# Performance work log

Hardware: AMD Instinct MI355X
Metric: run time of the kernel (lower is better)

The kernel has to match this reference:

```python
import jax, jax.numpy as jnp
import numpy as np

B, T, C = 4, 2048, 1024
H = 16
HS = C // H  # 64

def setup_inputs() -> dict:
    key = jax.random.key(0)
    k1, k2, k3, k4 = jax.random.split(key, 4)
    scale = 0.02
    return {
        "x": jax.random.normal(k1, (B, T, C), dtype=jnp.float32),
        "w_kqv": jax.random.normal(k2, (C, 3 * C), dtype=jnp.float32) * scale,
        "w_proj": jax.random.normal(k3, (C, C), dtype=jnp.float32) * scale,
        "b_proj": jax.random.normal(k4, (C,), dtype=jnp.float32) * scale,
    }

def reference(x, w_kqv, w_proj, b_proj):
    b, t, c = x.shape
    qkv = x @ w_kqv                       # [B,T,3C]
    q, k, v = jnp.split(qkv, 3, axis=-1)
    def heads(a):
        return a.reshape(b, t, H, HS).transpose(0, 2, 1, 3)  # [B,H,T,HS]
    q, k, v = heads(q), heads(k), heads(v)
    # faithful to source: scores MULTIPLIED by sqrt(head_size)
    scores = jnp.einsum('bhqd,bhkd->bhqk', q, k) * (HS ** 0.5)
    mask = jnp.tril(jnp.ones((t, t), dtype=bool))
    scores = jnp.where(mask[None, None], scores, -jnp.inf)
    attn = jax.nn.softmax(scores, axis=-1)
    out = jnp.einsum('bhqk,bhkd->bhqd', attn, v)  # [B,H,T,HS]
    out = out.transpose(0, 2, 1, 3).reshape(b, t, c)
    return out @ w_proj + b_proj
```

## Files before the change

### kernel.cpp

```cpp
#include <hip/hip_runtime.h>
#include <hip/hip_bf16.h>
#include <cstdint>

#define BB 4
#define TT 2048
#define CC 1024
#define HH 16
#define HS 64
#define MM (BB*TT)

#define QSCALE 11.5415603629f

typedef _Float16 f16;
typedef _Float16 f16x8 __attribute__((ext_vector_type(8)));
typedef _Float16 f16x4 __attribute__((ext_vector_type(4)));
typedef float f32x4 __attribute__((ext_vector_type(4)));
typedef float f32x16 __attribute__((ext_vector_type(16)));

#define MFMA16(a,b,c) __builtin_amdgcn_mfma_f32_16x16x32_f16(a,b,c,0,0,0)
#define MFMA32(a,b,c) __builtin_amdgcn_mfma_f32_32x32x16_f16(a,b,c,0,0,0)

__device__ __forceinline__ void g2lds16(void* lds, const void* g) {
  __builtin_amdgcn_global_load_lds(
      (const __attribute__((address_space(1))) void*)g,
      (__attribute__((address_space(3))) void*)lds, 16, 0, 0);
}

__device__ __forceinline__ int pk2(float a, float b) {
  auto r = __builtin_amdgcn_cvt_pkrtz(a, b);
  return __builtin_bit_cast(int, r);
}

union U8 { int4 i; f16x8 h; };

__global__ __launch_bounds__(256) void cvt_kernel(const float* __restrict__ in,
                                                  f16* __restrict__ out, int n4) {
  int i = blockIdx.x * blockDim.x + threadIdx.x;
  if (i < n4) {
    float4 v = ((const float4*)in)[i];
    f16x4 o;
    o[0] = (f16)v.x; o[1] = (f16)v.y; o[2] = (f16)v.z; o[3] = (f16)v.w;
    ((f16x4*)out)[i] = o;
  }
}

__global__ __launch_bounds__(256) void transpose_cvt(const float* __restrict__ in,
                                                     f16* __restrict__ out,
                                                     int K, int N) {
  __shared__ float tile[32][33];
  int n0 = blockIdx.x * 32, k0 = blockIdx.y * 32;
  int tx = threadIdx.x, ty = threadIdx.y;
  #pragma unroll
  for (int i = 0; i < 32; i += 8)
    tile[ty + i][tx] = in[(size_t)(k0 + ty + i) * N + n0 + tx];
  __syncthreads();
  #pragma unroll
  for (int i = 0; i < 32; i += 8)
    out[(size_t)(n0 + ty + i) * K + k0 + tx] = (f16)tile[tx][ty + i];
}

__device__ __forceinline__ void gstage(const f16* __restrict__ A,
                                       const f16* __restrict__ Bt,
                                       f16* as, f16* bs,
                                       int row0, int col0, int kt, int t) {
  const int K = 1024;
  #pragma unroll
  for (int i = 0; i < 2; ++i) {
    int off = i * 8192 + t * 16;
    int row = off >> 7;
    int cbB = off & 127;
    int scb = cbB ^ ((row & 7) << 4);
    g2lds16((char*)as + off, (const char*)(A  + (size_t)(row0 + row) * K + kt) + scb);
    g2lds16((char*)bs + off, (const char*)(Bt + (size_t)(col0 + row) * K + kt) + scb);
  }
}

template<int EPI>
__global__ __launch_bounds__(512) void gemm_bt(const f16* __restrict__ A,
                                               const f16* __restrict__ Bt,
                                               f16* __restrict__ qT,
                                               f16* __restrict__ kT,
                                               f16* __restrict__ vT,
                                               const float* __restrict__ bias,
                                               float* __restrict__ outF) {
  const int K = 1024;
  __shared__ f16 As[2][128 * 64];
  __shared__ f16 Bs[2][128 * 64];
  const int t = threadIdx.x;
  const int l = t & 63, w = t >> 6;
  const int lr = l & 15, lh = l >> 4;
  const int row0 = blockIdx.y * 128, col0 = blockIdx.x * 128;
  const int wm = w >> 2, wn = w & 3;
  const int wr = wm * 64, wc = wn * 32;
  const int sx = (lr & 7) << 4;

  f32x4 acc[4][2] = {};

  gstage(A, Bt, As[0], Bs[0], row0, col0, 0, t);
  int buf = 0;
  for (int kt = 0; kt < K; kt += 64) {
    asm volatile("" ::: "memory");
    const bool pf = (kt + 64) < K;
    if (pf) gstage(A, Bt, As[buf ^ 1], Bs[buf ^ 1], row0, col0, kt + 64, t);
    if (pf) asm volatile("s_waitcnt vmcnt(4)" ::: "memory");
    else    asm volatile("s_waitcnt vmcnt(0)" ::: "memory");
    __builtin_amdgcn_sched_barrier(0);
    __builtin_amdgcn_s_barrier();
    const char* as = (const char*)As[buf];
    const char* bs = (const char*)Bs[buf];
    __builtin_amdgcn_s_setprio(1);
    #pragma unroll
    for (int kk = 0; kk < 64; kk += 32) {
      f16x8 af[4], bfr[2];
      #pragma unroll
      for (int m = 0; m < 4; ++m)
        af[m]  = *(const f16x8*)(as + (wr + m * 16 + lr) * 128
                                    + ((kk * 2 + lh * 16) ^ sx));
      #pragma unroll
      for (int n = 0; n < 2; ++n)
        bfr[n] = *(const f16x8*)(bs + (wc + n * 16 + lr) * 128
                                    + ((kk * 2 + lh * 16) ^ sx));
      #pragma unroll
      for (int m = 0; m < 4; ++m)
        #pragma unroll
        for (int n = 0; n < 2; ++n)
          acc[m][n] = MFMA16(af[m], bfr[n], acc[m][n]);
    }
    __builtin_amdgcn_s_setprio(0);
    __builtin_amdgcn_sched_barrier(0);
    __builtin_amdgcn_s_barrier();
    buf ^= 1;
  }

  #pragma unroll
  for (int m = 0; m < 4; ++m) {
    #pragma unroll
    for (int n = 0; n < 2; ++n) {
      #pragma unroll
      for (int j = 0; j < 4; ++j) {
        float val = acc[m][n][j];
        int gr = row0 + wr + m * 16 + lh * 4 + j;
        int gc = col0 + wc + n * 16 + lr;
        if (EPI == 0) {
          int which = gc >> 10;
          int c = gc & 1023;
          int h = c >> 6, d = c & 63;
          int b = gr >> 11, tt = gr & 2047;
          size_t bh = (size_t)(b * HH + h);
          if (which == 0)      qT[(bh * TT + tt) * HS + d] = (f16)(val * QSCALE);
          else if (which == 1) kT[(bh * TT + tt) * HS + d] = (f16)val;
          else                 vT[(bh * HS + d) * TT + tt] = (f16)val;
        } else {
          outF[(size_t)gr * CC + gc] = val + bias[gc];
        }
      }
    }
  }
}

template<bool MASKED>
__device__ __forceinline__ void step32L(
    int kglob, int qa, int l31, int hi,
    const f16* __restrict__ ks, const f16* __restrict__ vs, int kbs,
    const f16x8 (&qf)[4],
    float& m, f32x4& lv, f32x16& oA, f32x16& oB) {
  const int sx = (l31 & 7) << 4;
  const char* krow = (const char*)(ks + (kbs + l31) * 64);
  f32x16 sa = {}, sb = {};
  {
    f16x8 kf0 = *(const f16x8*)(krow + ((0 * 32 + hi * 16) ^ sx));
    f16x8 kf1 = *(const f16x8*)(krow + ((1 * 32 + hi * 16) ^ sx));
    f16x8 kf2 = *(const f16x8*)(krow + ((2 * 32 + hi * 16) ^ sx));
    f16x8 kf3 = *(const f16x8*)(krow + ((3 * 32 + hi * 16) ^ sx));
    sa = MFMA32(kf0, qf[0], sa);
    sb = MFMA32(kf2, qf[2], sb);
    sa = MFMA32(kf1, qf[1], sa);
    sb = MFMA32(kf3, qf[3], sb);
  }
  float p[16];
  #pragma unroll
  for (int r = 0; r < 16; ++r) {
    float sv = sa[r] + sb[r];
    if (MASKED) {
      int k = kglob + (r & 3) + 8 * (r >> 2) + 4 * hi;
      p[r] = (k <= qa) ? sv : -INFINITY;
    } else p[r] = sv;
  }
  float t0 = fmaxf(fmaxf(p[0], p[1]), fmaxf(p[2], p[3]));
  float t1 = fmaxf(fmaxf(p[4], p[5]), fmaxf(p[6], p[7]));
  float t2 = fmaxf(fmaxf(p[8], p[9]), fmaxf(p[10], p[11]));
  float t3 = fmaxf(fmaxf(p[12], p[13]), fmaxf(p[14], p[15]));
  float mx = fmaxf(fmaxf(t0, t1), fmaxf(t2, t3));
  if (__any(mx > m + 14.0f)) {
    mx = fmaxf(mx, __shfl_xor(mx, 32));
    float mn = fmaxf(m, mx);
    float corr = __builtin_amdgcn_exp2f(m - mn);
    m = mn;
    #pragma unroll
    for (int r = 0; r < 4; ++r) lv[r] *= corr;
    #pragma unroll
    for (int r = 0; r < 16; ++r) { oA[r] *= corr; oB[r] *= corr; }
  }
  #pragma unroll
  for (int r = 0; r < 16; ++r) {
    p[r] = __builtin_amdgcn_exp2f(p[r] - m);
    lv[r & 3] += p[r];
  }
  int pkv[8];
  #pragma unroll
  for (int j = 0; j < 8; ++j) pkv[j] = pk2(p[2 * j], p[2 * j + 1]);
  int e0 = pkv[0], e2 = pkv[2];
  asm("v_permlane32_swap_b32 %0, %1" : "+v"(e0), "+v"(e2));
  int e1 = pkv[1], e3 = pkv[3];
  asm("v_permlane32_swap_b32 %0, %1" : "+v"(e1), "+v"(e3));
  int f0 = pkv[4], f2 = pkv[6];
  asm("v_permlane32_swap_b32 %0, %1" : "+v"(f0), "+v"(f2));
  int f1 = pkv[5], f3 = pkv[7];
  asm("v_permlane32_swap_b32 %0, %1" : "+v"(f1), "+v"(f3));
  U8 b0, b1;
  b0.i = (int4){ e0, e1, e2, e3 };
  b1.i = (int4){ f0, f1, f2, f3 };
  const char* vrow0 = (const char*)(vs + l31 * 64);
  const char* vrow1 = (const char*)(vs + (l31 + 32) * 64);
  const int kc0 = (kbs * 2 + hi * 16) ^ sx;
  const int kc1 = (kbs * 2 + hi * 16 + 32) ^ sx;
  f16x8 v00 = *(const f16x8*)(vrow0 + kc0);
  f16x8 v01 = *(const f16x8*)(vrow0 + kc1);
  f16x8 v10 = *(const f16x8*)(vrow1 + kc0);
  f16x8 v11 = *(const f16x8*)(vrow1 + kc1);
  oA = MFMA32(v00, b0.h, oA);
  oA = MFMA32(v01, b1.h, oA);
  oB = MFMA32(v10, b0.h, oB);
  oB = MFMA32(v11, b1.h, oB);
}

__device__ __forceinline__ void stage_tile(const f16* __restrict__ Kb,
                                           const f16* __restrict__ Vb,
                                           f16* ks, f16* vs,
                                           int kb, int w, int l) {
  #pragma unroll
  for (int j = 0; j < 2; ++j) {
    int off = w * 2048 + j * 1024 + l * 16;
    int row = off >> 7;
    int cb  = off & 127;
    int scb = cb ^ ((row & 7) << 4);
    g2lds16((char*)ks + off, (const char*)(Kb + (size_t)(kb + row) * HS) + scb);
    g2lds16((char*)vs + off, (const char*)(Vb + (size_t)row * TT + kb) + scb);
  }
}

__global__ __launch_bounds__(256) void attn_kernel(const f16* __restrict__ qT,
                                                   const f16* __restrict__ kT,
                                                   const f16* __restrict__ vT,
                                                   f16* __restrict__ aout) {
  const int bh = blockIdx.x;
  const int pr = blockIdx.y;
  const int t = threadIdx.x, l = t & 63, w = t >> 6;
  const int l31 = l & 31, hi = l >> 5;
  const f16* __restrict__ Qb = qT + (size_t)bh * TT * HS;
  const f16* __restrict__ Kb = kT + (size_t)bh * TT * HS;
  const f16* __restrict__ Vb = vT + (size_t)bh * HS * TT;
  const int b = bh >> 4, h = bh & 15;

  __shared__ f16 Ks[2][64 * 64];
  __shared__ f16 Vs[2][64 * 64];

  #pragma unroll
  for (int ph = 0; ph < 2; ++ph) {
    const int qb = ph ? pr : (15 - pr);
    const int q0w = qb * 128 + w * 32;
    const int qa = q0w + l31;

    f16x8 qf[4];
    #pragma unroll
    for (int j = 0; j < 4; ++j)
      qf[j] = *(const f16x8*)&Qb[(size_t)qa * HS + 16 * j + hi * 8];

    float m = -INFINITY;
    f32x4 lv = {};
    f32x16 oA = {}, oB = {};

    const int nt = 2 * qb + 2;
    stage_tile(Kb, Vb, Ks[0], Vs[0], 0, w, l);
    __syncthreads();
    int buf = 0;
    for (int ti = 0; ti < nt; ++ti) {
      if (ti + 1 < nt)
        stage_tile(Kb, Vb, Ks[buf ^ 1], Vs[buf ^ 1], (ti + 1) * 64, w, l);
      const int kb = ti * 64;
      const f16* ks = Ks[buf];
      const f16* vs = Vs[buf];
      if (kb < q0w)
        step32L<false>(kb, qa, l31, hi, ks, vs, 0, qf, m, lv, oA, oB);
      else if (kb == q0w)
        step32L<true >(kb, qa, l31, hi, ks, vs, 0, qf, m, lv, oA, oB);
      if (kb + 32 < q0w)
        step32L<false>(kb + 32, qa, l31, hi, ks, vs, 32, qf, m, lv, oA, oB);
      else if (kb + 32 == q0w)
        step32L<true >(kb + 32, qa, l31, hi, ks, vs, 32, qf, m, lv, oA, oB);
      __syncthreads();
      buf ^= 1;
    }

    float lsum = (lv[0] + lv[1]) + (lv[2] + lv[3]);
    lsum += __shfl_xor(lsum, 32);
    float li = 1.0f / lsum;

    f16* orow = aout + (size_t)(b * TT + qa) * CC + h * HS;
    #pragma unroll
    for (int rq = 0; rq < 4; ++rq) {
      f16x4 o4a, o4b;
      #pragma unroll
      for (int j = 0; j < 4; ++j) {
        int r = rq * 4 + j;
        o4a[j] = (f16)(oA[r] * li);
        o4b[j] = (f16)(oB[r] * li);
      }
      int dA = 8 * rq + 4 * hi;
      *(f16x4*)&orow[dA]      = o4a;
      *(f16x4*)&orow[32 + dA] = o4b;
    }
    __syncthreads();
  }
}

extern "C" void kernel_launch(void* const* d_in, const int* in_sizes, int n_in,
                              void* d_out, int out_size, void* d_ws, size_t ws_size,
                              hipStream_t stream) {
  const float* x      = (const float*)d_in[0];
  const float* w_kqv  = (const float*)d_in[1];
  const float* w_proj = (const float*)d_in[2];
  const float* b_proj = (const float*)d_in[3];
  float* out = (float*)d_out;

  char* ws = (char*)d_ws;
  f16* xb    = (f16*)(ws);
  f16* wkqvT = (f16*)(ws + 16777216);
  f16* wpT   = (f16*)(ws + 23068672);
  f16* qT    = (f16*)(ws + 25165824);
  f16* kT    = (f16*)(ws + 41943040);
  f16* vT    = (f16*)(ws + 58720256);
  f16* aout  = (f16*)(ws + 75497472);

  cvt_kernel<<<8192, 256, 0, stream>>>(x, xb, (MM * CC) / 4);
  transpose_cvt<<<dim3(3 * CC / 32, CC / 32), dim3(32, 8), 0, stream>>>(w_kqv, wkqvT, CC, 3 * CC);
  transpose_cvt<<<dim3(CC / 32, CC / 32), dim3(32, 8), 0, stream>>>(w_proj, wpT, CC, CC);

  gemm_bt<0><<<dim3(3 * CC / 128, MM / 128), 512, 0, stream>>>(xb, wkqvT, qT, kT, vT, nullptr, nullptr);

  attn_kernel<<<dim3(BB * HH, 8), 256, 0, stream>>>(qT, kT, vT, aout);

  gemm_bt<1><<<dim3(CC / 128, MM / 128), 512, 0, stream>>>(aout, wpT, nullptr, nullptr, nullptr, b_proj, out);
}
```

Before: 212.4 us.

## Split attention KV tiles across two wave groups and merge softmax partials in LDS

The attention kernel now runs 512 threads per block. Two groups of four waves each handle one 32-key half of every 64-key tile for the same query rows, and staging is split across all eight waves. At the end, the second group writes its partial output, max and sum to LDS, and the first group merges them flash-decoding style before writing. This doubles the waves per block to raise parallelism and latency hiding (the grid is only 512 blocks). In exchange it adds an LDS merge step, an extra barrier, and a shared union buffer.

```diff
diff --git a/kernel.cpp b/kernel.cpp
--- a/kernel.cpp
+++ b/kernel.cpp
@@ -234,41 +234,48 @@
   oB = MFMA32(v11, b1.h, oB);
 }
 
-__device__ __forceinline__ void stage_tile(const f16* __restrict__ Kb,
-                                           const f16* __restrict__ Vb,
-                                           f16* ks, f16* vs,
-                                           int kb, int w, int l) {
-  #pragma unroll
-  for (int j = 0; j < 2; ++j) {
-    int off = w * 2048 + j * 1024 + l * 16;
-    int row = off >> 7;
-    int cb  = off & 127;
-    int scb = cb ^ ((row & 7) << 4);
-    g2lds16((char*)ks + off, (const char*)(Kb + (size_t)(kb + row) * HS) + scb);
-    g2lds16((char*)vs + off, (const char*)(Vb + (size_t)row * TT + kb) + scb);
-  }
-}
-
-__global__ __launch_bounds__(256) void attn_kernel(const f16* __restrict__ qT,
+struct SmemU {
+  union {
+    f16 kv[2][2][4096];
+    float om[4][64][32];
+  };
+  float mls[4][64][2];
+};
+
+__device__ __forceinline__ void stage8(const f16* __restrict__ Kb,
+                                       const f16* __restrict__ Vb,
+                                       f16* ks, f16* vs,
+                                       int kb, int w, int l) {
+  int off = w * 1024 + l * 16;
+  int row = off >> 7;
+  int cb  = off & 127;
+  int scb = cb ^ ((row & 7) << 4);
+  g2lds16((char*)ks + off, (const char*)(Kb + (size_t)(kb + row) * HS) + scb);
+  g2lds16((char*)vs + off, (const char*)(Vb + (size_t)row * TT + kb) + scb);
+}
+
+__global__ __launch_bounds__(512) void attn_kernel(const f16* __restrict__ qT,
                                                    const f16* __restrict__ kT,
                                                    const f16* __restrict__ vT,
                                                    f16* __restrict__ aout) {
   const int bh = blockIdx.x;
   const int pr = blockIdx.y;
   const int t = threadIdx.x, l = t & 63, w = t >> 6;
+  const int ws = w & 3;
+  const int kh = w >> 2;
   const int l31 = l & 31, hi = l >> 5;
   const f16* __restrict__ Qb = qT + (size_t)bh * TT * HS;
   const f16* __restrict__ Kb = kT + (size_t)bh * TT * HS;
   const f16* __restrict__ Vb = vT + (size_t)bh * HS * TT;
   const int b = bh >> 4, h = bh & 15;
 
-  __shared__ f16 Ks[2][64 * 64];
-  __shared__ f16 Vs[2][64 * 64];
+  __shared__ SmemU S;
+  const int swm = (l & 7) << 2;
 
   #pragma unroll
   for (int ph = 0; ph < 2; ++ph) {
     const int qb = ph ? pr : (15 - pr);
-    const int q0w = qb * 128 + w * 32;
+    const int q0w = qb * 128 + ws * 32;
     const int qa = q0w + l31;
 
     f16x8 qf[4];
@@ -281,44 +288,68 @@
     f32x16 oA = {}, oB = {};
 
     const int nt = 2 * qb + 2;
-    stage_tile(Kb, Vb, Ks[0], Vs[0], 0, w, l);
+    stage8(Kb, Vb, S.kv[0][0], S.kv[0][1], 0, w, l);
     __syncthreads();
     int buf = 0;
     for (int ti = 0; ti < nt; ++ti) {
       if (ti + 1 < nt)
-        stage_tile(Kb, Vb, Ks[buf ^ 1], Vs[buf ^ 1], (ti + 1) * 64, w, l);
+        stage8(Kb, Vb, S.kv[buf ^ 1][0], S.kv[buf ^ 1][1], (ti + 1) * 64, w, l);
       const int kb = ti * 64;
-      const f16* ks = Ks[buf];
-      const f16* vs = Vs[buf];
-      if (kb < q0w)
-        step32L<false>(kb, qa, l31, hi, ks, vs, 0, qf, m, lv, oA, oB);
-      else if (kb == q0w)
-        step32L<true >(kb, qa, l31, hi, ks, vs, 0, qf, m, lv, oA, oB);
-      if (kb + 32 < q0w)
-        step32L<false>(kb + 32, qa, l31, hi, ks, vs, 32, qf, m, lv, oA, oB);
-      else if (kb + 32 == q0w)
-        step32L<true >(kb + 32, qa, l31, hi, ks, vs, 32, qf, m, lv, oA, oB);
+      const f16* ks = S.kv[buf][0];
+      const f16* vs = S.kv[buf][1];
+      if (kh == 0) {
+        if (kb < q0w)
+          step32L<false>(kb, qa, l31, hi, ks, vs, 0, qf, m, lv, oA, oB);
+        else if (kb == q0w)
+          step32L<true >(kb, qa, l31, hi, ks, vs, 0, qf, m, lv, oA, oB);
+      } else {
+        if (kb + 32 < q0w)
+          step32L<false>(kb + 32, qa, l31, hi, ks, vs, 32, qf, m, lv, oA, oB);
+        else if (kb + 32 == q0w)
+          step32L<true >(kb + 32, qa, l31, hi, ks, vs, 32, qf, m, lv, oA, oB);
+      }
       __syncthreads();
       buf ^= 1;
     }
 
     float lsum = (lv[0] + lv[1]) + (lv[2] + lv[3]);
     lsum += __shfl_xor(lsum, 32);
-    float li = 1.0f / lsum;
-
-    f16* orow = aout + (size_t)(b * TT + qa) * CC + h * HS;
-    #pragma unroll
-    for (int rq = 0; rq < 4; ++rq) {
-      f16x4 o4a, o4b;
-      #pragma unroll
-      for (int j = 0; j < 4; ++j) {
-        int r = rq * 4 + j;
-        o4a[j] = (f16)(oA[r] * li);
-        o4b[j] = (f16)(oB[r] * li);
+
+    if (kh == 1) {
+      #pragma unroll
+      for (int rb = 0; rb < 4; ++rb) {
+        f32x4 va = { oA[rb*4+0], oA[rb*4+1], oA[rb*4+2], oA[rb*4+3] };
+        f32x4 vb = { oB[rb*4+0], oB[rb*4+1], oB[rb*4+2], oB[rb*4+3] };
+        *(f32x4*)&S.om[ws][l][(rb * 4) ^ swm]        = va;
+        *(f32x4*)&S.om[ws][l][((4 + rb) * 4) ^ swm]  = vb;
       }
-      int dA = 8 * rq + 4 * hi;
-      *(f16x4*)&orow[dA]      = o4a;
-      *(f16x4*)&orow[32 + dA] = o4b;
+      S.mls[ws][l][0] = m;
+      S.mls[ws][l][1] = lsum;
+    }
+    __syncthreads();
+    if (kh == 0) {
+      float mB = S.mls[ws][l][0], lB = S.mls[ws][l][1];
+      float mS = fmaxf(fmaxf(m, mB), -3.0e38f);
+      float cA = __builtin_amdgcn_exp2f(m - mS);
+      float cB = __builtin_amdgcn_exp2f(mB - mS);
+      float li = 1.0f / (lsum * cA + lB * cB);
+      float sA = cA * li, sB = cB * li;
+      f16* orow = aout + (size_t)(b * TT + qa) * CC + h * HS;
+      #pragma unroll
+      for (int rq = 0; rq < 4; ++rq) {
+        f32x4 obl = *(const f32x4*)&S.om[ws][l][(rq * 4) ^ swm];
+        f32x4 obh = *(const f32x4*)&S.om[ws][l][((4 + rq) * 4) ^ swm];
+        f16x4 o4a, o4b;
+        #pragma unroll
+        for (int j = 0; j < 4; ++j) {
+          int r = rq * 4 + j;
+          o4a[j] = (f16)(oA[r] * sA + obl[j] * sB);
+          o4b[j] = (f16)(oB[r] * sA + obh[j] * sB);
+        }
+        int dA = 8 * rq + 4 * hi;
+        *(f16x4*)&orow[dA]      = o4a;
+        *(f16x4*)&orow[32 + dA] = o4b;
+      }
     }
     __syncthreads();
   }
@@ -348,7 +379,7 @@
 
   gemm_bt<0><<<dim3(3 * CC / 128, MM / 128), 512, 0, stream>>>(xb, wkqvT, qT, kT, vT, nullptr, nullptr);
 
-  attn_kernel<<<dim3(BB * HH, 8), 256, 0, stream>>>(qT, kT, vT, aout);
+  attn_kernel<<<dim3(BB * HH, 8), 512, 0, stream>>>(qT, kT, vT, aout);
 
   gemm_bt<1><<<dim3(CC / 128, MM / 128), 512, 0, stream>>>(aout, wpT, nullptr, nullptr, nullptr, b_proj, out);
 }
```

After: 191.0 us. 1.11x faster.
